# Kernel tuning notes

Hardware: AMD Instinct MI355X
Metric: run time of the kernel (lower is better)

Reference implementation:

```python
import jax, jax.numpy as jnp
import numpy as np

N = 128  # padded Hadamard size (find_min_power(122))
H1 = W1 = 122

def _hadamard(n):
    H = np.array([[1.0]], dtype=np.float32)
    while H.shape[0] < n:
        H = np.block([[H, H], [H, -H]])
    return H

_H = jnp.asarray(_hadamard(N))  # symmetric 128x128 +/-1 matrix
_DN = ('NCHW', 'OIHW', 'NCHW')

def _conv(x, w, b, stride, pad):
    y = jax.lax.conv_general_dilated(x, w, (stride, stride),
                                     [(pad, pad), (pad, pad)], dimension_numbers=_DN)
    return y + b[None, :, None, None]

def _convT(x, w, b, stride, pad):
    # torch ConvTranspose2d weight layout [in, out, kh, kw]
    k = w.shape[-1]
    wf = jnp.flip(w, (2, 3)).transpose(1, 0, 2, 3)  # -> [out, in, kh, kw]
    p = k - 1 - pad
    y = jax.lax.conv_general_dilated(x, wf, (1, 1), [(p, p), (p, p)],
                                     lhs_dilation=(stride, stride), dimension_numbers=_DN)
    return y + b[None, :, None, None]

def _fwht2(x):
    # fwht along -1 then -2 (dense Hadamard matmul, matching fast=False path)
    x = jnp.einsum('bchw,wk->bchk', x, _H)
    return jnp.einsum('bchw,hk->bckw', x, _H)

def _ifwht2(x):
    x = jnp.einsum('bchw,wk->bchk', x, _H) / N
    return jnp.einsum('bchw,hk->bckw', x, _H) / N

def _pad(x):
    return jnp.pad(x, ((0, 0), (0, 0), (0, N - H1), (0, N - W1)))

def _thresh(x, T):
    aT = jnp.abs(T)
    s = jnp.copysign(jax.nn.relu(jnp.abs(x) - aT), x)
    return s + jnp.sign(s) * aT

def _kl(q):
    e = q.size // 64
    p = jax.nn.sigmoid(jnp.full((64,), 0.001, q.dtype))
    qm = jnp.sum(jax.nn.sigmoid(jnp.abs(q).reshape(e, 64)), axis=0) / e
    return jnp.sum(p * jnp.log(p / qm)) + jnp.sum((1 - p) * jnp.log((1 - p) / (1 - qm)))

def _tv(x, weight):
    b, c, h, w = x.shape
    tv = jnp.abs(x[:, :, 1:, :] - x[:, :, :-1, :]).sum() + \
         jnp.abs(x[:, :, :, 1:] - x[:, :, :, :-1]).sum()
    return weight * tv / (b * c * h * w)

def setup_inputs() -> dict:
    key = jax.random.key(0)
    ks = jax.random.split(key, 16)
    B = 128
    inp = {
        'x': jax.random.normal(ks[0], (B, 1, 256, 256), jnp.float32),
        'val': 0,
        'v1': jax.random.uniform(ks[1], (N, N), jnp.float32),
        'T1': jax.random.uniform(ks[2], (N, N), jnp.float32) / 10,
        'v2': jax.random.uniform(ks[3], (N, N), jnp.float32),
        'T2': jax.random.uniform(ks[4], (N, N), jnp.float32) / 10,
        'v3': jax.random.uniform(ks[5], (N, N), jnp.float32),
        'T3': jax.random.uniform(ks[6], (N, N), jnp.float32) / 10,
        'w1': jax.random.normal(ks[7], (4, 1, 16, 16), jnp.float32) * 0.05,
        'b1': jax.random.normal(ks[8], (4,), jnp.float32) * 0.01,
        'w2': jax.random.normal(ks[9], (4, 4, 7, 7), jnp.float32) * 0.05,
        'b2': jax.random.normal(ks[10], (4,), jnp.float32) * 0.01,
        'w3': jax.random.normal(ks[11], (4, 4, 7, 7), jnp.float32) * 0.05,  # [in,out,kh,kw]
        'b3': jax.random.normal(ks[12], (4,), jnp.float32) * 0.01,
        'w4': jax.random.normal(ks[13], (4, 1, 16, 16), jnp.float32) * 0.05,  # [in,out,kh,kw]
        'b4': jax.random.normal(ks[14], (1,), jnp.float32) * 0.01,
    }
    return inp

def reference(x, val, v1, T1, v2, T2, v3, T3, w1, b1, w2, b2, w3, b3, w4, b4):
    TV_WEIGHT = 0.05  # original draws np.random.uniform(0, 0.1); fixed for determinism
    x1 = _conv(x, w1, b1, 2, 1)                       # [B,4,122,122]
    x6 = _thresh(v1 * _fwht2(_pad(x1)), T1)           # [B,4,128,128]
    x9 = _ifwht2(x6)[..., :H1, :W1]
    x10 = _conv(x9, w2, b2, 1, 3)                     # [B,4,122,122]
    x15 = _thresh(v2 * _fwht2(_pad(x10)), T2)
    x18 = _ifwht2(x15)[..., :H1, :W1]
    x19 = _convT(x18, w3, b3, 1, 3) + x10
    x24 = _thresh(v3 * _fwht2(_pad(x19)), T3)
    x27 = _ifwht2(x24 + x6)[..., :H1, :W1]
    out = _convT(x27, w4, b4, 2, 1) * x               # [B,1,256,256]
    loss = 1.0 * _tv(out, TV_WEIGHT) + 0.1 * (_kl(x6) + _kl(x15) + _kl(x24))
    return out, loss
```

## Files before the change

### kernel.cpp

```cpp
#include <hip/hip_runtime.h>
#include <math.h>

#define PLANE 16384
#define NPLANES 512

__device__ __forceinline__ void had64(float* __restrict__ v) {
#pragma unroll
    for (int m = 1; m <= 32; m <<= 1) {
#pragma unroll
        for (int r = 0; r < 64; ++r) {
            if (!(r & m)) {
                int s = r | m;
                float a = v[r], b = v[s];
                v[r] = a + b; v[s] = a - b;
            }
        }
    }
}

__device__ __forceinline__ void bit6x(float* __restrict__ v, float sg) {
#pragma unroll
    for (int j = 0; j < 64; ++j) {
        float p = __shfl_xor(v[j], 1);
        v[j] = fmaf(sg, v[j], p);
    }
}

#define LPITCH 132

template <bool ADDPOST>
__global__ __launch_bounds__(256) void fwht_kernel_t(
    const float* __restrict__ in, const float* __restrict__ vmat,
    const float* __restrict__ tmat, const float* __restrict__ addbuf,
    float* __restrict__ outInv, float* __restrict__ klpart)
{
    __shared__ float lds[128 * LPITCH];
    const int t = threadIdx.x;
    const int r = t >> 1;
    const int hf = t & 1;
    const float sg = hf ? -1.f : 1.f;
    const int plane = blockIdx.x;
    const float* src = in + (size_t)plane * PLANE;

    float v[64];
#pragma unroll
    for (int k = 0; k < 16; ++k)
        *(float4*)&v[4 * k] = *(const float4*)&src[r * 128 + hf * 64 + 4 * k];

    had64(v); bit6x(v, sg);

#pragma unroll
    for (int k = 0; k < 16; ++k)
        *(float4*)&lds[r * LPITCH + hf * 64 + 4 * k] = *(const float4*)&v[4 * k];
    __syncthreads();
#pragma unroll
    for (int j = 0; j < 64; ++j)
        v[j] = lds[(hf * 64 + j) * LPITCH + r];

    had64(v); bit6x(v, sg);

    float ls = 0.f;
#pragma unroll
    for (int j = 0; j < 64; ++j) {
        int idx = (hf * 64 + j) * 128 + r;
        float y = v[j] * vmat[idx];
        float tt = fabsf(tmat[idx]);
        y = (fabsf(y) > tt) ? y : 0.f;
        ls += 1.f / (1.f + __expf(-fabsf(y)));
        v[j] = y;
    }
    ls += __shfl_xor(ls, 1);
    {
        int W = t >> 6;
        if (hf == 0)
            klpart[(size_t)(plane * 2 + (W >> 1)) * 64 + (r & 63)] = ls;
    }

    had64(v); bit6x(v, sg);

    __syncthreads();
#pragma unroll
    for (int j = 0; j < 64; ++j)
        lds[(hf * 64 + j) * LPITCH + r] = v[j];
    __syncthreads();
#pragma unroll
    for (int k = 0; k < 16; ++k)
        *(float4*)&v[4 * k] = *(const float4*)&lds[r * LPITCH + hf * 64 + 4 * k];

    had64(v); bit6x(v, sg);

    float* dst = outInv + (size_t)plane * PLANE;
    const float s = 1.f / 16384.f;
    bool rowv = r < 122;
#pragma unroll
    for (int k = 0; k < 16; ++k) {
        int wb = hf * 64 + 4 * k;
        int rowoff = r * 128 + wb;
        float4 ad = make_float4(0.f, 0.f, 0.f, 0.f);
        if (ADDPOST) ad = *(const float4*)&addbuf[(size_t)plane * PLANE + rowoff];
        float4 o;
        o.x = (rowv && wb + 0 < 122) ? fmaf(v[4 * k],     s, ad.x) : 0.f;
        o.y = (rowv && wb + 1 < 122) ? fmaf(v[4 * k + 1], s, ad.y) : 0.f;
        o.z = (rowv && wb + 2 < 122) ? fmaf(v[4 * k + 2], s, ad.z) : 0.f;
        o.w = (rowv && wb + 3 < 122) ? fmaf(v[4 * k + 3], s, ad.w) : 0.f;
        *(float4*)&dst[rowoff] = o;
    }
}

__global__ void prep_weights(const float* __restrict__ w3, const float* __restrict__ w4,
                             float* __restrict__ w3c, float* __restrict__ w4p)
{
    int tid = blockIdx.x * 256 + threadIdx.x;
    if (tid < 784) {
        int oc = tid / 196;
        int rem = tid - oc * 196;
        int ic = rem / 49;
        int k = rem - ic * 49;
        int kh = k / 7, kw = k - kh * 7;
        w3c[(oc * 4 + ic) * 49 + k] = w3[(ic * 4 + oc) * 49 + (6 - kh) * 7 + (6 - kw)];
    }
    if (tid < 1024) {
        int u = tid & 7, t = (tid >> 3) & 7, pb = (tid >> 6) & 1, pa = (tid >> 7) & 1, ic = tid >> 8;
        int kh = 2 * t + (pa ? 0 : 1);
        int kw = 2 * u + (pb ? 0 : 1);
        w4p[tid] = w4[ic * 256 + kh * 16 + kw];
    }
}

__global__ __launch_bounds__(256) void conv1_kernel(
    const float* __restrict__ x, const float* __restrict__ w1,
    const float* __restrict__ b1, float* __restrict__ out)
{
    __shared__ float tile[78][80];
    int tx = blockIdx.x, ty = blockIdx.y, b = blockIdx.z;
    int tid = threadIdx.x;
    const float* xp = x + (size_t)b * 65536;
    int r0g = ty * 64 - 1, c0g = tx * 64 - 1;
    for (int i = tid; i < 78 * 78; i += 256) {
        int rr = i / 78, cc = i - rr * 78;
        int gi = r0g + rr, gj = c0g + cc;
        tile[rr][cc] = (gi >= 0 && gi < 256 && gj >= 0 && gj < 256) ? xp[gi * 256 + gj] : 0.f;
    }
    __syncthreads();
    int cg = tid & 7, r = tid >> 3;
    int B = cg * 4;
    float acc[4][4];
#pragma unroll
    for (int oc = 0; oc < 4; ++oc)
#pragma unroll
        for (int c = 0; c < 4; ++c) acc[oc][c] = 0.f;
#pragma unroll 1
    for (int kh = 0; kh < 16; ++kh) {
        float win[24];
        const float* trow = &tile[2 * r + kh][2 * B];
#pragma unroll
        for (int k = 0; k < 6; ++k)
            *(float4*)&win[4 * k] = *(const float4*)&trow[4 * k];
#pragma unroll
        for (int oc = 0; oc < 4; ++oc) {
            const float* wr = w1 + oc * 256 + kh * 16;
#pragma unroll
            for (int kw = 0; kw < 16; ++kw) {
                float wv = wr[kw];
#pragma unroll
                for (int c = 0; c < 4; ++c)
                    acc[oc][c] = fmaf(win[2 * c + kw], wv, acc[oc][c]);
            }
        }
    }
    int oh = ty * 32 + r;
    int owb = tx * 32 + B;
    bool rowv = oh < 122;
#pragma unroll
    for (int oc = 0; oc < 4; ++oc) {
        float bv = b1[oc];
        float4 res;
        res.x = (rowv && owb + 0 < 122) ? acc[oc][0] + bv : 0.f;
        res.y = (rowv && owb + 1 < 122) ? acc[oc][1] + bv : 0.f;
        res.z = (rowv && owb + 2 < 122) ? acc[oc][2] + bv : 0.f;
        res.w = (rowv && owb + 3 < 122) ? acc[oc][3] + bv : 0.f;
        *(float4*)&out[(((size_t)b * 4 + oc) << 14) + (oh << 7) + owb] = res;
    }
}

__global__ __launch_bounds__(256) void conv7_kernel(
    const float* __restrict__ in, const float* __restrict__ w,
    const float* __restrict__ bias, const float* __restrict__ skip,
    float* __restrict__ out)
{
    __shared__ float tile[4][38][40];
    int tx = blockIdx.x, ty = blockIdx.y, b = blockIdx.z;
    int tid = threadIdx.x;
    int r0g = ty * 32 - 3, c0g = tx * 32 - 3;
    for (int i = tid; i < 4 * 38 * 38; i += 256) {
        int ic = i / 1444;
        int rem = i - ic * 1444;
        int rr = rem / 38, cc = rem - rr * 38;
        int gi = r0g + rr, gj = c0g + cc;
        float v = 0.f;
        if (gi >= 0 && gi < 128 && gj >= 0 && gj < 128)
            v = in[(((size_t)b * 4 + ic) << 14) + (gi << 7) + gj];
        tile[ic][rr][cc] = v;
    }
    __syncthreads();
    int cg = tid & 7, r = tid >> 3;
    int B = cg * 4;
    float acc[4][4];
#pragma unroll
    for (int oc = 0; oc < 4; ++oc)
#pragma unroll
        for (int c = 0; c < 4; ++c) acc[oc][c] = 0.f;
#pragma unroll 1
    for (int ic = 0; ic < 4; ++ic) {
#pragma unroll 1
        for (int kh = 0; kh < 7; ++kh) {
            float win[12];
            const float* trow = &tile[ic][r + kh][B];
#pragma unroll
            for (int k = 0; k < 3; ++k)
                *(float4*)&win[4 * k] = *(const float4*)&trow[4 * k];
#pragma unroll
            for (int oc = 0; oc < 4; ++oc) {
                const float* wr = w + (oc * 4 + ic) * 49 + kh * 7;
#pragma unroll
                for (int kw = 0; kw < 7; ++kw) {
                    float wv = wr[kw];
#pragma unroll
                    for (int c = 0; c < 4; ++c)
                        acc[oc][c] = fmaf(win[c + kw], wv, acc[oc][c]);
                }
            }
        }
    }
    int oh = ty * 32 + r;
    int owb = tx * 32 + B;
    bool rowv = oh < 122;
#pragma unroll
    for (int oc = 0; oc < 4; ++oc) {
        size_t o = (((size_t)b * 4 + oc) << 14) + (oh << 7) + owb;
        float4 sv = make_float4(0.f, 0.f, 0.f, 0.f);
        if (skip) sv = *(const float4*)&skip[o];
        float bv = bias[oc];
        float4 res;
        res.x = (rowv && owb + 0 < 122) ? acc[oc][0] + bv + sv.x : 0.f;
        res.y = (rowv && owb + 1 < 122) ? acc[oc][1] + bv + sv.y : 0.f;
        res.z = (rowv && owb + 2 < 122) ? acc[oc][2] + bv + sv.z : 0.f;
        res.w = (rowv && owb + 3 < 122) ? acc[oc][3] + bv + sv.w : 0.f;
        *(float4*)&out[o] = res;
    }
}

#define CT_HALF(T, ROW, PA)                                                    \
    _Pragma("unroll")                                                          \
    for (int pb = 0; pb < 2; ++pb) {                                           \
        const float* w8 = wp + (((ic * 2 + (PA)) * 2 + pb) * 8 + (T)) * 8;     \
        _Pragma("unroll")                                                      \
        for (int u = 0; u < 8; ++u) {                                          \
            float wv = w8[u];                                                  \
            _Pragma("unroll")                                                  \
            for (int c = 0; c < 4; ++c)                                        \
                acc[PA][pb][c] = fmaf(ROW[8 + c + pb - u], wv, acc[PA][pb][c]);\
        }                                                                      \
    }

__global__ __launch_bounds__(256) void convt4_kernel(
    const float* __restrict__ in, const float* __restrict__ wp,
    const float* __restrict__ bias, const float* __restrict__ xin,
    float* __restrict__ out)
{
    __shared__ float tile[4][40][44];
    int tx = blockIdx.x, ty = blockIdx.y, b = blockIdx.z;
    int tid = threadIdx.x;
    int A0 = ty * 32, B0 = tx * 32;
    int r0g = A0 - 7, c0g = B0 - 8;
    for (int i = tid; i < 4 * 40 * 44; i += 256) {
        int ic = i / 1760;
        int rem = i - ic * 1760;
        int rr = rem / 44, cc = rem - rr * 44;
        int gi = r0g + rr, gj = c0g + cc;
        float v = 0.f;
        if (gi >= 0 && gi < 128 && gj >= 0 && gj < 128)
            v = in[(((size_t)b * 4 + ic) << 14) + (gi << 7) + gj];
        tile[ic][rr][cc] = v;
    }
    __syncthreads();
    int cg = tid & 7, ra = tid >> 3;
    float acc[2][2][4];
#pragma unroll
    for (int pa = 0; pa < 2; ++pa)
#pragma unroll
        for (int pb = 0; pb < 2; ++pb)
#pragma unroll
            for (int c = 0; c < 4; ++c) acc[pa][pb][c] = 0.f;
#pragma unroll 1
    for (int ic = 0; ic < 4; ++ic) {
        float bufA[16], bufB[16];
#pragma unroll
        for (int k = 0; k < 4; ++k)
            *(float4*)&bufB[4 * k] = *(const float4*)&tile[ic][ra + 8][4 * cg + 4 * k];
#pragma unroll 1
        for (int t2 = 0; t2 < 8; t2 += 2) {
#pragma unroll
            for (int k = 0; k < 4; ++k)
                *(float4*)&bufA[4 * k] = *(const float4*)&tile[ic][ra + 7 - t2][4 * cg + 4 * k];
            CT_HALF(t2, bufA, 0)
            CT_HALF(t2, bufB, 1)
#pragma unroll
            for (int k = 0; k < 4; ++k)
                *(float4*)&bufB[4 * k] = *(const float4*)&tile[ic][ra + 6 - t2][4 * cg + 4 * k];
            CT_HALF(t2 + 1, bufB, 0)
            CT_HALF(t2 + 1, bufA, 1)
        }
    }
    int oh0 = 2 * (A0 + ra);
    int owb = 2 * (B0 + 4 * cg);
    float bv = bias[0];
#pragma unroll
    for (int pa = 0; pa < 2; ++pa) {
        size_t o = (size_t)b * 65536 + (size_t)(oh0 + pa) * 256 + owb;
        float4 x0 = *(const float4*)&xin[o];
        float4 x1 = *(const float4*)&xin[o + 4];
        float4 r0, r1;
        r0.x = (acc[pa][0][0] + bv) * x0.x;
        r0.y = (acc[pa][1][0] + bv) * x0.y;
        r0.z = (acc[pa][0][1] + bv) * x0.z;
        r0.w = (acc[pa][1][1] + bv) * x0.w;
        r1.x = (acc[pa][0][2] + bv) * x1.x;
        r1.y = (acc[pa][1][2] + bv) * x1.y;
        r1.z = (acc[pa][0][3] + bv) * x1.z;
        r1.w = (acc[pa][1][3] + bv) * x1.w;
        *(float4*)&out[o] = r0;
        *(float4*)&out[o + 4] = r1;
    }
}

__global__ __launch_bounds__(256) void tv_kernel(
    const float* __restrict__ out, float* __restrict__ tvpart)
{
    const float4* out4 = (const float4*)out;
    __shared__ float red[256];
    int tid = threadIdx.x;
    float local = 0.f;
    const int total4 = 128 * 65536 / 4;
    for (int i4 = blockIdx.x * 256 + tid; i4 < total4; i4 += gridDim.x * 256) {
        float4 a = out4[i4];
        int i = i4 << 2;
        local += fabsf(a.y - a.x) + fabsf(a.z - a.y) + fabsf(a.w - a.z);
        if ((i & 255) != 252) local += fabsf(out[i + 4] - a.w);
        if ((i & 65535) < 65280) {
            float4 c = out4[i4 + 64];
            local += fabsf(c.x - a.x) + fabsf(c.y - a.y) + fabsf(c.z - a.z) + fabsf(c.w - a.w);
        }
    }
    red[tid] = local;
    __syncthreads();
    for (int s = 128; s > 0; s >>= 1) {
        if (tid < s) red[tid] += red[tid + s];
        __syncthreads();
    }
    if (tid == 0) tvpart[blockIdx.x] = red[0];
}

__global__ __launch_bounds__(256) void reduce1_kernel(
    const float* __restrict__ klpart, const float* __restrict__ tvpart,
    float* __restrict__ klred, float* __restrict__ tvred)
{
    int bid = blockIdx.x;
    int tid = threadIdx.x;
    if (bid < 48) {
        int layer = bid >> 4, chunk = bid & 15;
        int sub = tid >> 6, t = tid & 63;
        const float* base = klpart + (size_t)layer * 65536 + (size_t)chunk * 64 * 64;
        float s = 0.f;
        for (int r = sub; r < 64; r += 4)
            s += base[r * 64 + t];
        __shared__ float red[4][64];
        red[sub][t] = s;
        __syncthreads();
        if (tid < 64)
            klred[(layer * 16 + chunk) * 64 + tid] =
                red[0][tid] + red[1][tid] + red[2][tid] + red[3][tid];
    } else {
        __shared__ float red[256];
        float s = 0.f;
        for (int i = tid; i < 2048; i += 256) s += tvpart[i];
        red[tid] = s;
        __syncthreads();
        for (int st = 128; st > 0; st >>= 1) {
            if (tid < st) red[tid] += red[tid + st];
            __syncthreads();
        }
        if (tid == 0) tvred[0] = red[0];
    }
}

__global__ __launch_bounds__(64) void finalize2_kernel(
    const float* __restrict__ klred, const float* __restrict__ tvred,
    float* __restrict__ lossout)
{
    int t = threadIdx.x;
    float p = 1.f / (1.f + __expf(-0.001f));
    float term = 0.f;
#pragma unroll
    for (int l = 0; l < 3; ++l) {
        float q = 0.f;
#pragma unroll
        for (int c = 0; c < 16; ++c)
            q += klred[(l * 16 + c) * 64 + t];
        float qm = q * (1.f / 131072.f);
        term += p * logf(p / qm) + (1.f - p) * logf((1.f - p) / (1.f - qm));
    }
#pragma unroll
    for (int off = 32; off > 0; off >>= 1)
        term += __shfl_down(term, off);
    if (t == 0)
        lossout[0] = 0.05f * tvred[0] / 8388608.f + 0.1f * term;
}

extern "C" void kernel_launch(void* const* d_in, const int* in_sizes, int n_in,
                              void* d_out, int out_size, void* d_ws, size_t ws_size,
                              hipStream_t stream) {
    (void)in_sizes; (void)n_in; (void)out_size; (void)ws_size;
    const float* x  = (const float*)d_in[0];
    const float* v1 = (const float*)d_in[2];
    const float* T1 = (const float*)d_in[3];
    const float* v2 = (const float*)d_in[4];
    const float* T2 = (const float*)d_in[5];
    const float* v3 = (const float*)d_in[6];
    const float* T3 = (const float*)d_in[7];
    const float* w1 = (const float*)d_in[8];
    const float* b1 = (const float*)d_in[9];
    const float* w2 = (const float*)d_in[10];
    const float* b2 = (const float*)d_in[11];
    const float* w3 = (const float*)d_in[12];
    const float* b3 = (const float*)d_in[13];
    const float* w4 = (const float*)d_in[14];
    const float* b4 = (const float*)d_in[15];
    float* out = (float*)d_out;

    float* W0 = (float*)d_ws;
    float* W1 = W0 + (size_t)NPLANES * PLANE;
    float* W2 = W1 + (size_t)NPLANES * PLANE;
    float* klpart = W2 + (size_t)NPLANES * PLANE;
    float* tvpart = klpart + 3 * 1024 * 64;
    float* klred  = tvpart + 2048;
    float* tvred  = klred + 3072;
    float* w3c = tvred + 64;
    float* w4p = w3c + 784;
    float* x10buf = out;

    prep_weights<<<4, 256, 0, stream>>>(w3, w4, w3c, w4p);
    conv1_kernel<<<dim3(4, 4, 128), 256, 0, stream>>>(x, w1, b1, W0);
    fwht_kernel_t<false><<<NPLANES, 256, 0, stream>>>(W0, v1, T1, nullptr, W1, klpart);
    conv7_kernel<<<dim3(4, 4, 128), 256, 0, stream>>>(W1, w2, b2, nullptr, x10buf);
    fwht_kernel_t<false><<<NPLANES, 256, 0, stream>>>(x10buf, v2, T2, nullptr, W0, klpart + 65536);
    conv7_kernel<<<dim3(4, 4, 128), 256, 0, stream>>>(W0, w3c, b3, x10buf, W2);
    fwht_kernel_t<true><<<NPLANES, 256, 0, stream>>>(W2, v3, T3, W1, W0, klpart + 2 * 65536);
    convt4_kernel<<<dim3(4, 4, 128), 256, 0, stream>>>(W0, w4p, b4, x, out);
    tv_kernel<<<2048, 256, 0, stream>>>(out, tvpart);
    reduce1_kernel<<<49, 256, 0, stream>>>(klpart, tvpart, klred, tvred);
    finalize2_kernel<<<1, 64, 0, stream>>>(klred, tvred, out + 8388608);
}
```

Before: 412.6 us.

## Replace butterfly Hadamard transforms with split-bf16 MFMA matmuls

The register/shuffle butterfly FWHT kernel is replaced by dense 128x128 Hadamard matmuls on MFMA bf16 instructions. Each operand is split into hi/lo bf16 parts to keep near-fp32 accuracy, and the Hadamard matrix is built as bf16 in a prep kernel. Intermediate transposes go through LDS, and the KL partial layout and its reduction are adjusted to match. This moves the work from VALU to matrix cores, but it adds 2x MFMA work, extra LDS traffic and rounding error from the bf16 split. The epilogue also changes from float4 stores to scalar ones.

```diff
diff --git a/kernel.cpp b/kernel.cpp
--- a/kernel.cpp
+++ b/kernel.cpp
@@ -3,112 +3,196 @@
 
 #define PLANE 16384
 #define NPLANES 512
-
-__device__ __forceinline__ void had64(float* __restrict__ v) {
-#pragma unroll
-    for (int m = 1; m <= 32; m <<= 1) {
-#pragma unroll
-        for (int r = 0; r < 64; ++r) {
-            if (!(r & m)) {
-                int s = r | m;
-                float a = v[r], b = v[s];
-                v[r] = a + b; v[s] = a - b;
-            }
-        }
-    }
-}
-
-__device__ __forceinline__ void bit6x(float* __restrict__ v, float sg) {
-#pragma unroll
-    for (int j = 0; j < 64; ++j) {
-        float p = __shfl_xor(v[j], 1);
-        v[j] = fmaf(sg, v[j], p);
-    }
-}
-
-#define LPITCH 132
+#define MP 136
+
+typedef __attribute__((ext_vector_type(8))) short bf16x8;
+typedef __attribute__((ext_vector_type(4))) float f32x4;
+typedef __attribute__((ext_vector_type(4))) unsigned short ushort4v;
+
+__device__ __forceinline__ unsigned short f2bf(float x) {
+    union { float f; unsigned u; } a; a.f = x;
+    unsigned r = a.u + 0x7FFFu + ((a.u >> 16) & 1u);
+    return (unsigned short)(r >> 16);
+}
+__device__ __forceinline__ float bf2f(unsigned short h) {
+    union { unsigned u; float f; } a; a.u = ((unsigned)h) << 16;
+    return a.f;
+}
+__device__ __forceinline__ void split_bf16(float x, unsigned short& hi, unsigned short& lo) {
+    hi = f2bf(x);
+    lo = f2bf(x - bf2f(hi));
+}
+
+__device__ __forceinline__ void mm_pass(const unsigned short* __restrict__ Hg,
+                                        const unsigned short* __restrict__ Mhi,
+                                        const unsigned short* __restrict__ Mlo,
+                                        f32x4 acc[2][8], int wv, int l)
+{
+    const int lr = l & 15, lg = l >> 4;
+#pragma unroll
+    for (int m = 0; m < 2; ++m)
+#pragma unroll
+        for (int n = 0; n < 8; ++n)
+            acc[m][n] = f32x4{0.f, 0.f, 0.f, 0.f};
+#pragma unroll 1
+    for (int kk = 0; kk < 4; ++kk) {
+        bf16x8 ahi[2], alo[2];
+#pragma unroll
+        for (int m = 0; m < 2; ++m) {
+            int row = wv * 32 + m * 16 + lr;
+            int off = row * MP + kk * 32 + lg * 8;
+            ahi[m] = *(const bf16x8*)&Mhi[off];
+            alo[m] = *(const bf16x8*)&Mlo[off];
+        }
+#pragma unroll
+        for (int n = 0; n < 8; ++n) {
+            int col = n * 16 + lr;
+            bf16x8 b = *(const bf16x8*)&Hg[col * 128 + kk * 32 + lg * 8];
+#pragma unroll
+            for (int m = 0; m < 2; ++m) {
+                acc[m][n] = __builtin_amdgcn_mfma_f32_16x16x32_bf16(ahi[m], b, acc[m][n], 0, 0, 0);
+                acc[m][n] = __builtin_amdgcn_mfma_f32_16x16x32_bf16(alo[m], b, acc[m][n], 0, 0, 0);
+            }
+        }
+    }
+}
 
 template <bool ADDPOST>
-__global__ __launch_bounds__(256) void fwht_kernel_t(
+__global__ __launch_bounds__(256) void fwht_mfma_t(
     const float* __restrict__ in, const float* __restrict__ vmat,
     const float* __restrict__ tmat, const float* __restrict__ addbuf,
+    const unsigned short* __restrict__ Hg,
     float* __restrict__ outInv, float* __restrict__ klpart)
 {
-    __shared__ float lds[128 * LPITCH];
-    const int t = threadIdx.x;
-    const int r = t >> 1;
-    const int hf = t & 1;
-    const float sg = hf ? -1.f : 1.f;
+    __shared__ unsigned short Mhi[128 * MP];
+    __shared__ unsigned short Mlo[128 * MP];
+    const int tid = threadIdx.x;
+    const int wv = tid >> 6, l = tid & 63;
+    const int lr = l & 15, lg = l >> 4;
     const int plane = blockIdx.x;
-    const float* src = in + (size_t)plane * PLANE;
-
-    float v[64];
-#pragma unroll
-    for (int k = 0; k < 16; ++k)
-        *(float4*)&v[4 * k] = *(const float4*)&src[r * 128 + hf * 64 + 4 * k];
-
-    had64(v); bit6x(v, sg);
-
-#pragma unroll
-    for (int k = 0; k < 16; ++k)
-        *(float4*)&lds[r * LPITCH + hf * 64 + 4 * k] = *(const float4*)&v[4 * k];
-    __syncthreads();
-#pragma unroll
-    for (int j = 0; j < 64; ++j)
-        v[j] = lds[(hf * 64 + j) * LPITCH + r];
-
-    had64(v); bit6x(v, sg);
-
-    float ls = 0.f;
-#pragma unroll
-    for (int j = 0; j < 64; ++j) {
-        int idx = (hf * 64 + j) * 128 + r;
-        float y = v[j] * vmat[idx];
-        float tt = fabsf(tmat[idx]);
-        y = (fabsf(y) > tt) ? y : 0.f;
-        ls += 1.f / (1.f + __expf(-fabsf(y)));
-        v[j] = y;
-    }
-    ls += __shfl_xor(ls, 1);
-    {
-        int W = t >> 6;
-        if (hf == 0)
-            klpart[(size_t)(plane * 2 + (W >> 1)) * 64 + (r & 63)] = ls;
-    }
-
-    had64(v); bit6x(v, sg);
-
-    __syncthreads();
-#pragma unroll
-    for (int j = 0; j < 64; ++j)
-        lds[(hf * 64 + j) * LPITCH + r] = v[j];
-    __syncthreads();
-#pragma unroll
-    for (int k = 0; k < 16; ++k)
-        *(float4*)&v[4 * k] = *(const float4*)&lds[r * LPITCH + hf * 64 + 4 * k];
-
-    had64(v); bit6x(v, sg);
-
+
+    const float4* src4 = (const float4*)(in + (size_t)plane * PLANE);
+#pragma unroll
+    for (int g = 0; g < 16; ++g) {
+        int i4 = g * 256 + tid;
+        float4 x = src4[i4];
+        int base = i4 << 2;
+        int row = base >> 7, col = base & 127;
+        unsigned short h0, h1, h2, h3, o0, o1, o2, o3;
+        split_bf16(x.x, h0, o0); split_bf16(x.y, h1, o1);
+        split_bf16(x.z, h2, o2); split_bf16(x.w, h3, o3);
+        *(ushort4v*)&Mhi[row * MP + col] = ushort4v{h0, h1, h2, h3};
+        *(ushort4v*)&Mlo[row * MP + col] = ushort4v{o0, o1, o2, o3};
+    }
+    __syncthreads();
+
+    f32x4 acc[2][8];
+
+    mm_pass(Hg, Mhi, Mlo, acc, wv, l);
+    __syncthreads();
+#pragma unroll
+    for (int m = 0; m < 2; ++m)
+#pragma unroll
+        for (int n = 0; n < 8; ++n)
+#pragma unroll
+            for (int i = 0; i < 4; ++i) {
+                unsigned short hi, lo;
+                split_bf16(acc[m][n][i], hi, lo);
+                int rs = wv * 32 + m * 16 + lg * 4 + i;
+                int cs = n * 16 + lr;
+                Mhi[cs * MP + rs] = hi; Mlo[cs * MP + rs] = lo;
+            }
+    __syncthreads();
+
+    mm_pass(Hg, Mhi, Mlo, acc, wv, l);
+    float ls[2][4];
+#pragma unroll
+    for (int m = 0; m < 2; ++m)
+#pragma unroll
+        for (int i = 0; i < 4; ++i) ls[m][i] = 0.f;
+#pragma unroll
+    for (int n = 0; n < 8; ++n) {
+        int h = n * 16 + lr;
+#pragma unroll
+        for (int m = 0; m < 2; ++m)
+#pragma unroll
+            for (int i = 0; i < 4; ++i) {
+                int w = wv * 32 + m * 16 + lg * 4 + i;
+                float vv = vmat[h * 128 + w];
+                float tt = fabsf(tmat[h * 128 + w]);
+                float y = acc[m][n][i] * vv;
+                y = (fabsf(y) > tt) ? y : 0.f;
+                ls[m][i] += 1.f / (1.f + __expf(-fabsf(y)));
+                acc[m][n][i] = y;
+            }
+    }
+#pragma unroll
+    for (int m = 0; m < 2; ++m)
+#pragma unroll
+        for (int i = 0; i < 4; ++i) {
+            float s = ls[m][i];
+            s += __shfl_xor(s, 1); s += __shfl_xor(s, 2);
+            s += __shfl_xor(s, 4); s += __shfl_xor(s, 8);
+            ls[m][i] = s;
+        }
+    if (lr == 0) {
+#pragma unroll
+        for (int m = 0; m < 2; ++m)
+#pragma unroll
+            for (int i = 0; i < 4; ++i)
+                klpart[(size_t)plane * 128 + wv * 32 + m * 16 + lg * 4 + i] = ls[m][i];
+    }
+    __syncthreads();
+#pragma unroll
+    for (int m = 0; m < 2; ++m)
+#pragma unroll
+        for (int n = 0; n < 8; ++n)
+#pragma unroll
+            for (int i = 0; i < 4; ++i) {
+                unsigned short hi, lo;
+                split_bf16(acc[m][n][i], hi, lo);
+                int rs = wv * 32 + m * 16 + lg * 4 + i;
+                int cs = n * 16 + lr;
+                Mhi[rs * MP + cs] = hi; Mlo[rs * MP + cs] = lo;
+            }
+    __syncthreads();
+
+    mm_pass(Hg, Mhi, Mlo, acc, wv, l);
+    __syncthreads();
+#pragma unroll
+    for (int m = 0; m < 2; ++m)
+#pragma unroll
+        for (int n = 0; n < 8; ++n)
+#pragma unroll
+            for (int i = 0; i < 4; ++i) {
+                unsigned short hi, lo;
+                split_bf16(acc[m][n][i], hi, lo);
+                int rs = wv * 32 + m * 16 + lg * 4 + i;
+                int cs = n * 16 + lr;
+                Mhi[cs * MP + rs] = hi; Mlo[cs * MP + rs] = lo;
+            }
+    __syncthreads();
+
+    mm_pass(Hg, Mhi, Mlo, acc, wv, l);
     float* dst = outInv + (size_t)plane * PLANE;
-    const float s = 1.f / 16384.f;
-    bool rowv = r < 122;
-#pragma unroll
-    for (int k = 0; k < 16; ++k) {
-        int wb = hf * 64 + 4 * k;
-        int rowoff = r * 128 + wb;
-        float4 ad = make_float4(0.f, 0.f, 0.f, 0.f);
-        if (ADDPOST) ad = *(const float4*)&addbuf[(size_t)plane * PLANE + rowoff];
-        float4 o;
-        o.x = (rowv && wb + 0 < 122) ? fmaf(v[4 * k],     s, ad.x) : 0.f;
-        o.y = (rowv && wb + 1 < 122) ? fmaf(v[4 * k + 1], s, ad.y) : 0.f;
-        o.z = (rowv && wb + 2 < 122) ? fmaf(v[4 * k + 2], s, ad.z) : 0.f;
-        o.w = (rowv && wb + 3 < 122) ? fmaf(v[4 * k + 3], s, ad.w) : 0.f;
-        *(float4*)&dst[rowoff] = o;
-    }
+    const float sc = 1.f / 16384.f;
+#pragma unroll
+    for (int m = 0; m < 2; ++m)
+#pragma unroll
+        for (int n = 0; n < 8; ++n)
+#pragma unroll
+            for (int i = 0; i < 4; ++i) {
+                int rs = wv * 32 + m * 16 + lg * 4 + i;
+                int cs = n * 16 + lr;
+                float val = acc[m][n][i] * sc;
+                if (ADDPOST) val += addbuf[(size_t)plane * PLANE + rs * 128 + cs];
+                dst[rs * 128 + cs] = (rs < 122 && cs < 122) ? val : 0.f;
+            }
 }
 
 __global__ void prep_weights(const float* __restrict__ w3, const float* __restrict__ w4,
-                             float* __restrict__ w3c, float* __restrict__ w4p)
+                             float* __restrict__ w3c, float* __restrict__ w4p,
+                             unsigned short* __restrict__ Hg)
 {
     int tid = blockIdx.x * 256 + threadIdx.x;
     if (tid < 784) {
@@ -124,6 +208,10 @@
         int kh = 2 * t + (pa ? 0 : 1);
         int kw = 2 * u + (pb ? 0 : 1);
         w4p[tid] = w4[ic * 256 + kh * 16 + kw];
+    }
+    if (tid < 16384) {
+        int i = tid >> 7, j = tid & 127;
+        Hg[tid] = (__popc(i & j) & 1) ? 0xBF80u : 0x3F80u;
     }
 }
 
@@ -370,10 +458,12 @@
     if (bid < 48) {
         int layer = bid >> 4, chunk = bid & 15;
         int sub = tid >> 6, t = tid & 63;
-        const float* base = klpart + (size_t)layer * 65536 + (size_t)chunk * 64 * 64;
+        const float* base = klpart + (size_t)layer * 65536;
         float s = 0.f;
-        for (int r = sub; r < 64; r += 4)
-            s += base[r * 64 + t];
+        for (int p = sub; p < 32; p += 4) {
+            const float* r = base + (size_t)(chunk * 32 + p) * 128;
+            s += r[t] + r[64 + t];
+        }
         __shared__ float red[4][64];
         red[sub][t] = s;
         __syncthreads();
@@ -442,20 +532,21 @@
     float* W1 = W0 + (size_t)NPLANES * PLANE;
     float* W2 = W1 + (size_t)NPLANES * PLANE;
     float* klpart = W2 + (size_t)NPLANES * PLANE;
-    float* tvpart = klpart + 3 * 1024 * 64;
+    float* tvpart = klpart + 3 * 512 * 128;
     float* klred  = tvpart + 2048;
     float* tvred  = klred + 3072;
     float* w3c = tvred + 64;
     float* w4p = w3c + 784;
+    unsigned short* Hg = (unsigned short*)(w4p + 1024);
     float* x10buf = out;
 
-    prep_weights<<<4, 256, 0, stream>>>(w3, w4, w3c, w4p);
+    prep_weights<<<64, 256, 0, stream>>>(w3, w4, w3c, w4p, Hg);
     conv1_kernel<<<dim3(4, 4, 128), 256, 0, stream>>>(x, w1, b1, W0);
-    fwht_kernel_t<false><<<NPLANES, 256, 0, stream>>>(W0, v1, T1, nullptr, W1, klpart);
+    fwht_mfma_t<false><<<NPLANES, 256, 0, stream>>>(W0, v1, T1, nullptr, Hg, W1, klpart);
     conv7_kernel<<<dim3(4, 4, 128), 256, 0, stream>>>(W1, w2, b2, nullptr, x10buf);
-    fwht_kernel_t<false><<<NPLANES, 256, 0, stream>>>(x10buf, v2, T2, nullptr, W0, klpart + 65536);
+    fwht_mfma_t<false><<<NPLANES, 256, 0, stream>>>(x10buf, v2, T2, nullptr, Hg, W0, klpart + 65536);
     conv7_kernel<<<dim3(4, 4, 128), 256, 0, stream>>>(W0, w3c, b3, x10buf, W2);
-    fwht_kernel_t<true><<<NPLANES, 256, 0, stream>>>(W2, v3, T3, W1, W0, klpart + 2 * 65536);
+    fwht_mfma_t<true><<<NPLANES, 256, 0, stream>>>(W2, v3, T3, W1, Hg, W0, klpart + 2 * 65536);
     convt4_kernel<<<dim3(4, 4, 128), 256, 0, stream>>>(W0, w4p, b4, x, out);
     tv_kernel<<<2048, 256, 0, stream>>>(out, tvpart);
     reduce1_kernel<<<49, 256, 0, stream>>>(klpart, tvpart, klred, tvred);
```

Result: slower. 447.3 us (+8.4%).
